# Kernel optimization log

Hardware: AMD Instinct MI355X
Metric: run time of the kernel (lower is better)

## Reference

```python
import jax, jax.numpy as jnp
import numpy as np

N = 50000      # nodes
E = 800000     # edges
FEAT = 128     # node_feat_size
HID = 128      # hidden_channels
LAT = 64       # latent_size
G = 256        # number of graphs in the batch


def _glorot_like(key, fan_in, shape):
    s = 1.0 / np.sqrt(fan_in)
    return jax.random.uniform(key, shape, jnp.float32, -s, s)


def setup_inputs() -> dict:
    key = jax.random.key(0)
    ks = jax.random.split(key, 13)
    x = jax.random.normal(ks[0], (N, FEAT), jnp.float32)
    edge_index = jax.random.randint(ks[1], (2, E), 0, N, dtype=jnp.int64)
    batch = jnp.sort(jax.random.randint(ks[2], (N,), 0, G, dtype=jnp.int64))
    return {
        "x": x,
        "edge_index": edge_index,
        "batch": batch,
        # GCNConv1: FEAT -> HID
        "W1": _glorot_like(ks[3], FEAT, (FEAT, HID)), "b1": jnp.zeros((HID,), jnp.float32),
        # GCNConv2: HID -> HID
        "W2": _glorot_like(ks[4], HID, (HID, HID)), "b2": jnp.zeros((HID,), jnp.float32),
        # fc: HID -> LAT
        "fcW": _glorot_like(ks[5], HID, (HID, LAT)), "fcb": _glorot_like(ks[6], HID, (LAT,)),
        # decoder: LAT -> HID
        "decW": _glorot_like(ks[7], LAT, (LAT, HID)), "decb": _glorot_like(ks[8], LAT, (HID,)),
        # GCNConv3: HID -> FEAT
        "W3": _glorot_like(ks[9], HID, (HID, FEAT)), "b3": jnp.zeros((FEAT,), jnp.float32),
    }


def reference(x, edge_index, batch, W1, b1, W2, b2, fcW, fcb, decW, decb, W3, b3):
    # --- GCN normalization with self-loops (computed once, shared by all convs) ---
    loop = jnp.arange(N, dtype=edge_index.dtype)
    row = jnp.concatenate([edge_index[0], loop])   # source nodes [E+N]
    col = jnp.concatenate([edge_index[1], loop])   # target nodes [E+N]
    deg = jax.ops.segment_sum(jnp.ones(row.shape, x.dtype), col, num_segments=N)
    dinv = jnp.where(deg > 0, jax.lax.rsqrt(deg), jnp.zeros_like(deg))
    norm = dinv[row] * dinv[col]                   # [E+N]

    def gcn(h, W, b):
        h = h @ W                                   # [N, out] transform first (PyG order)
        msg = h[row] * norm[:, None]                # gather + scale, [E+N, out]
        out = jax.ops.segment_sum(msg, col, num_segments=N)  # scatter-add
        return out + b

    # --- encode ---
    h = jax.nn.relu(gcn(x, W1, b1))
    h = jax.nn.relu(gcn(h, W2, b2))
    pooled = jax.ops.segment_sum(h, batch, num_segments=G)   # global_add_pool [G, HID]
    latent = jax.nn.relu(pooled @ fcW + fcb)                 # [G, LAT]

    # --- decode ---
    z = jax.nn.relu(latent @ decW + decb)                    # [G, HID]
    z = z[batch]                                             # broadcast back to nodes [N, HID]
    recon = gcn(z, W3, b3)                                   # [N, FEAT]
    return recon, latent
```

## Files before the change

### kernel.cpp

```cpp
#include <hip/hip_runtime.h>
#include <hip/hip_fp16.h>

static constexpr int NN   = 50000;
static constexpr int EE   = 800000;
static constexpr int GG   = 256;
static constexpr int PCH  = 16;
static constexpr int BK   = 128;
static constexpr int NB   = (NN + BK - 1) / BK;
static constexpr int CAP  = 4096;
static constexpr int CH   = 2048;
static constexpr int ABLK = (EE + CH - 1) / CH;

typedef _Float16 f16;
typedef f16  f16x8 __attribute__((ext_vector_type(8)));
typedef float f32x4 __attribute__((ext_vector_type(4)));

__device__ __forceinline__ int lowerb(const int* __restrict__ b, int n, int v) {
    int lo = 0, hi = n;
    while (lo < hi) { int m = (lo + hi) >> 1; if (b[m] < v) lo = m + 1; else hi = m; }
    return lo;
}

__global__ __launch_bounds__(256) void prep_k(const float* __restrict__ W1,
                                              const float* __restrict__ W2,
                                              f16x8* __restrict__ whi1, f16x8* __restrict__ wlo1,
                                              f16x8* __restrict__ whi2, f16x8* __restrict__ wlo2,
                                              int* __restrict__ bcur,
                                              float* __restrict__ pooled)
{
    int blk = blockIdx.x, t = threadIdx.x;
    if (blk < 16) {
        const float* W = (blk < 8) ? W1 : W2;
        f16x8* wh = (blk < 8) ? whi1 : whi2;
        f16x8* wl = (blk < 8) ? wlo1 : wlo2;
        int tid = (blk & 7) * 256 + t;
        int m  = tid & 15;
        int kq = (tid >> 4) & 3;
        int ks = (tid >> 6) & 3;
        int nt = tid >> 8;
        int n  = nt * 16 + m;
        int k0 = ks * 32 + kq * 8;
        f16x8 h8, l8;
        #pragma unroll
        for (int u = 0; u < 8; u++) {
            float x = W[(size_t)(k0 + u) * 128 + n];
            f16 h = (f16)x;
            h8[u] = h;
            l8[u] = (f16)(x - (float)h);
        }
        wh[tid] = h8;
        wl[tid] = l8;
    } else if (blk == 16) {
        for (int b = t; b < NB; b += 256) bcur[b] = b * CAP;
    } else {
        float4* p = (float4*)pooled;
        for (int j = (blk - 17) * 256 + t; j < GG * 32; j += 512)
            p[j] = make_float4(0.f, 0.f, 0.f, 0.f);
    }
}

__global__ __launch_bounds__(512) void binA_k(const int* __restrict__ ei,
                                              int* __restrict__ bcur,
                                              int2* __restrict__ eraw)
{
    __shared__ int2  stage[CH];
    __shared__ short sbid[CH];
    __shared__ int   hist[NB], loff[NB], gbase[NB], lcur[NB];
    __shared__ int   sc[512];

    int tid = threadIdx.x;
    int e0 = blockIdx.x * CH;
    int n = EE - e0; if (n > CH) n = CH;

    for (int b = tid; b < NB; b += 512) hist[b] = 0;
    __syncthreads();

    int2 r[CH / 512];
    #pragma unroll
    for (int k = 0; k < CH / 512; k++) {
        int s = k * 512 + tid;
        if (s < n) {
            int src = ei[e0 + s];
            int dst = ei[EE + e0 + s];
            r[k] = make_int2(src, dst);
            atomicAdd(&hist[dst >> 7], 1);
        }
    }
    __syncthreads();
    int v = (tid < NB) ? hist[tid] : 0;
    sc[tid] = v;
    __syncthreads();
    #pragma unroll
    for (int off = 1; off < 512; off <<= 1) {
        int add = (tid >= off) ? sc[tid - off] : 0;
        __syncthreads();
        sc[tid] += add;
        __syncthreads();
    }
    if (tid < NB) { int ex = sc[tid] - v; loff[tid] = ex; lcur[tid] = ex; }
    __syncthreads();
    for (int b = tid; b < NB; b += 512)
        gbase[b] = atomicAdd(&bcur[b], hist[b]);
    __syncthreads();
    #pragma unroll
    for (int k = 0; k < CH / 512; k++) {
        int s = k * 512 + tid;
        if (s < n) {
            int b = r[k].y >> 7;
            int slot = atomicAdd(&lcur[b], 1);
            stage[slot] = r[k];
            sbid[slot]  = (short)b;
        }
    }
    __syncthreads();
    for (int s = tid; s < n; s += 512) {
        int b = sbid[s];
        eraw[(size_t)gbase[b] + (s - loff[b])] = stage[s];
    }
}

__global__ __launch_bounds__(512) void scanb2_k(const int* __restrict__ bcur,
                                                int* __restrict__ bbase,
                                                int* __restrict__ rowptr)
{
    __shared__ int s[512];
    int t = threadIdx.x;
    int v = (t < NB) ? (bcur[t] - t * CAP) : 0;
    s[t] = v;
    __syncthreads();
    #pragma unroll
    for (int off = 1; off < 512; off <<= 1) {
        int add = (t >= off) ? s[t - off] : 0;
        __syncthreads();
        s[t] += add;
        __syncthreads();
    }
    if (t < NB) bbase[t] = s[t] - v;
    if (t == 0) rowptr[NN] = EE;
}

__global__ __launch_bounds__(512) void binB_k(const int2* __restrict__ eraw,
                                              const int* __restrict__ bcur,
                                              const int* __restrict__ bbase,
                                              int* __restrict__ rowptr,
                                              float* __restrict__ dinv,
                                              int* __restrict__ ebuf)
{
    __shared__ int hist[BK], excl[BK], cur[BK];
    int b = blockIdx.x, tid = threadIdx.x;
    int t0 = b << 7;
    int lim = NN - t0; if (lim > BK) lim = BK;
    int tot  = bcur[b] - b * CAP;
    int base = bbase[b];
    const int2* er = eraw + (size_t)b * CAP;

    if (tid < BK) hist[tid] = 0;
    __syncthreads();
    for (int s = tid; s < tot; s += 512) atomicAdd(&hist[er[s].y & 127], 1);
    __syncthreads();
    if (tid < BK) excl[tid] = hist[tid];
    __syncthreads();
    #pragma unroll
    for (int off = 1; off < BK; off <<= 1) {
        int add = (tid >= off && tid < BK) ? excl[tid - off] : 0;
        __syncthreads();
        if (tid < BK) excl[tid] += add;
        __syncthreads();
    }
    if (tid < BK) {
        int ex = excl[tid] - hist[tid];
        cur[tid] = base + ex;
        if (tid < lim) {
            rowptr[t0 + tid] = base + ex;
            dinv[t0 + tid]   = rsqrtf((float)(hist[tid] + 1));
        }
    }
    __syncthreads();
    for (int s = tid; s < tot; s += 512) {
        int2 rec = er[s];
        int p = atomicAdd(&cur[rec.y & 127], 1);
        ebuf[p] = rec.x;
    }
}

__global__ void pbb_k(const int* __restrict__ ebuf, const int* __restrict__ batch,
                      const float* __restrict__ dinv, int2* __restrict__ ebuf2)
{
    int e = blockIdx.x * 256 + threadIdx.x;
    if (e < EE) {
        int src = ebuf[e];
        ebuf2[e] = make_int2(batch[src], __float_as_int(dinv[src]));
    }
}

__global__ __launch_bounds__(256) void gemm_mfma3_k(const float* __restrict__ in,
                                                    const f16x8* __restrict__ whi_f,
                                                    const f16x8* __restrict__ wlo_f,
                                                    const float* __restrict__ dinv,
                                                    __half* __restrict__ out,
                                                    int rows)
{
    __shared__ __align__(16) f16x8 sh[2048];
    int tid  = threadIdx.x;
    #pragma unroll
    for (int u = 0; u < 8; u++) sh[u * 256 + tid] = whi_f[u * 256 + tid];
    __syncthreads();

    int lane = tid & 63;
    int wv   = tid >> 6;
    int rB   = blockIdx.x * 64 + wv * 16;
    int m    = lane & 15;
    int kq   = lane >> 4;
    int r    = rB + m;
    int rr   = (r < rows) ? r : (rows - 1);

    f16x8 ahi[4], alo[4];
    const float* rp = in + (size_t)rr * 128 + kq * 8;
    #pragma unroll
    for (int ks = 0; ks < 4; ks++) {
        float4 p0 = *(const float4*)(rp + ks * 32);
        float4 p1 = *(const float4*)(rp + ks * 32 + 4);
        float xs[8] = {p0.x, p0.y, p0.z, p0.w, p1.x, p1.y, p1.z, p1.w};
        #pragma unroll
        for (int u = 0; u < 8; u++) {
            f16 h = (f16)xs[u];
            ahi[ks][u] = h;
            alo[ks][u] = (f16)(xs[u] - (float)h);
        }
    }

    f32x4 acc[8];
    #pragma unroll
    for (int n = 0; n < 8; n++) acc[n] = (f32x4){0.f, 0.f, 0.f, 0.f};

    #pragma unroll
    for (int nt = 0; nt < 8; nt++) {
        #pragma unroll
        for (int ks = 0; ks < 4; ks++) {
            int idx = ((nt * 4 + ks) * 4 + kq) * 16 + m;
            f16x8 bh = sh[idx];
            f16x8 bl = wlo_f[idx];
            acc[nt] = __builtin_amdgcn_mfma_f32_16x16x32_f16(ahi[ks], bh, acc[nt], 0, 0, 0);
            acc[nt] = __builtin_amdgcn_mfma_f32_16x16x32_f16(alo[ks], bh, acc[nt], 0, 0, 0);
            acc[nt] = __builtin_amdgcn_mfma_f32_16x16x32_f16(ahi[ks], bl, acc[nt], 0, 0, 0);
        }
    }

    int   orow[4];
    float dv[4];
    #pragma unroll
    for (int j = 0; j < 4; j++) {
        int gr = rB + kq * 4 + j;
        orow[j] = gr;
        dv[j]   = (gr < rows) ? dinv[gr] : 0.f;
    }
    #pragma unroll
    for (int nt = 0; nt < 8; nt++) {
        int c = nt * 16 + m;
        #pragma unroll
        for (int j = 0; j < 4; j++) {
            if (orow[j] < rows)
                out[(size_t)orow[j] * 128 + c] = __float2half(acc[nt][j] * dv[j]);
        }
    }
}

__device__ __forceinline__ float4 gat4h(const __half* __restrict__ t, int s, int q)
{
    uint2 v = *(const uint2*)(t + ((size_t)s << 7) + q * 4);
    __half2 a = __builtin_bit_cast(__half2, v.x);
    __half2 b = __builtin_bit_cast(__half2, v.y);
    float2 fa = __half22float2(a), fb = __half22float2(b);
    return make_float4(fa.x, fa.y, fb.x, fb.y);
}

__global__ __launch_bounds__(64) void aggh_k(const __half* __restrict__ t,
                                             const int* __restrict__ rowptr,
                                             const int* __restrict__ ebuf,
                                             const float* __restrict__ dinv,
                                             const float* __restrict__ bias,
                                             float* __restrict__ out,
                                             int relu)
{
    int i    = blockIdx.x;
    int lane = threadIdx.x;
    int half = lane >> 5;
    int q    = lane & 31;

    int e0 = __builtin_amdgcn_readfirstlane(rowptr[i]);
    int e1 = __builtin_amdgcn_readfirstlane(rowptr[i + 1]);
    int deg = e1 - e0;
    int idxsafe = (deg > 0) ? (e0 + min(lane, deg - 1)) : 0;
    int myidx = ebuf[idxsafe];

    float a0 = 0.f, a1 = 0.f, a2 = 0.f, a3 = 0.f;
    if (half == 0) {
        float4 v = gat4h(t, i, q);
        a0 = v.x; a1 = v.y; a2 = v.z; a3 = v.w;
    }

    int v   = min(deg, 64);
    int c16 = v & ~15;
    for (int j = half * 8; j < c16; j += 16) {
        int s0 = __shfl(myidx, j + 0), s1 = __shfl(myidx, j + 1);
        int s2 = __shfl(myidx, j + 2), s3 = __shfl(myidx, j + 3);
        int s4 = __shfl(myidx, j + 4), s5 = __shfl(myidx, j + 5);
        int s6 = __shfl(myidx, j + 6), s7 = __shfl(myidx, j + 7);
        float4 w0 = gat4h(t, s0, q);
        float4 w1 = gat4h(t, s1, q);
        float4 w2 = gat4h(t, s2, q);
        float4 w3 = gat4h(t, s3, q);
        float4 w4 = gat4h(t, s4, q);
        float4 w5 = gat4h(t, s5, q);
        float4 w6 = gat4h(t, s6, q);
        float4 w7 = gat4h(t, s7, q);
        a0 += w0.x + w1.x + w2.x + w3.x + w4.x + w5.x + w6.x + w7.x;
        a1 += w0.y + w1.y + w2.y + w3.y + w4.y + w5.y + w6.y + w7.y;
        a2 += w0.z + w1.z + w2.z + w3.z + w4.z + w5.z + w6.z + w7.z;
        a3 += w0.w + w1.w + w2.w + w3.w + w4.w + w5.w + w6.w + w7.w;
    }
    if (v - c16 >= 8) {
        int j = c16 + half * 4;
        int s0 = __shfl(myidx, j + 0), s1 = __shfl(myidx, j + 1);
        int s2 = __shfl(myidx, j + 2), s3 = __shfl(myidx, j + 3);
        float4 w0 = gat4h(t, s0, q);
        float4 w1 = gat4h(t, s1, q);
        float4 w2 = gat4h(t, s2, q);
        float4 w3 = gat4h(t, s3, q);
        a0 += w0.x + w1.x + w2.x + w3.x;
        a1 += w0.y + w1.y + w2.y + w3.y;
        a2 += w0.z + w1.z + w2.z + w3.z;
        a3 += w0.w + w1.w + w2.w + w3.w;
    }
    int done = c16 + ((v - c16) & 8);
    for (int j = done + half; j < v; j += 2) {
        int s = __shfl(myidx, j);
        float4 w = gat4h(t, s, q);
        a0 += w.x; a1 += w.y; a2 += w.z; a3 += w.w;
    }
    for (int e = e0 + 64 + half; e < e1; e += 2) {
        float4 w = gat4h(t, ebuf[e], q);
        a0 += w.x; a1 += w.y; a2 += w.z; a3 += w.w;
    }

    a0 += __shfl_xor(a0, 32);
    a1 += __shfl_xor(a1, 32);
    a2 += __shfl_xor(a2, 32);
    a3 += __shfl_xor(a3, 32);

    if (half == 0) {
        float di = dinv[i];
        float4 b = *(const float4*)(bias + q * 4);
        float4 o;
        o.x = di * a0 + b.x;
        o.y = di * a1 + b.y;
        o.z = di * a2 + b.z;
        o.w = di * a3 + b.w;
        if (relu) {
            o.x = fmaxf(o.x, 0.f); o.y = fmaxf(o.y, 0.f);
            o.z = fmaxf(o.z, 0.f); o.w = fmaxf(o.w, 0.f);
        }
        *(float4*)(out + (size_t)i * 128 + q * 4) = o;
    }
}

__global__ __launch_bounds__(64) void agg_out_k(const float* __restrict__ zz,
                                                const int* __restrict__ batch,
                                                const int* __restrict__ rowptr,
                                                const int2* __restrict__ ebuf2,
                                                const float* __restrict__ dinv,
                                                const float* __restrict__ bias,
                                                float* __restrict__ out)
{
    int i    = blockIdx.x;
    int lane = threadIdx.x;
    int half = lane >> 5;
    int q    = lane & 31;
    float di = dinv[i];

    float a0 = 0.f, a1 = 0.f, a2 = 0.f, a3 = 0.f;
    if (half == 0) {
        float4 v = *(const float4*)(zz + ((size_t)batch[i] << 7) + q * 4);
        a0 = di * v.x; a1 = di * v.y; a2 = di * v.z; a3 = di * v.w;
    }

    int e0 = rowptr[i], e1 = rowptr[i + 1];
    int deg = e1 - e0;
    int full = deg & ~7;
    int ee = e0 + full;
    for (int e = e0 + half * 4; e < ee; e += 8) {
        int2 r0 = ebuf2[e],     r1 = ebuf2[e + 1];
        int2 r2 = ebuf2[e + 2], r3 = ebuf2[e + 3];
        float4 w0 = *(const float4*)(zz + ((size_t)r0.x << 7) + q * 4);
        float4 w1 = *(const float4*)(zz + ((size_t)r1.x << 7) + q * 4);
        float4 w2 = *(const float4*)(zz + ((size_t)r2.x << 7) + q * 4);
        float4 w3 = *(const float4*)(zz + ((size_t)r3.x << 7) + q * 4);
        float n0 = __int_as_float(r0.y), n1 = __int_as_float(r1.y);
        float n2 = __int_as_float(r2.y), n3 = __int_as_float(r3.y);
        a0 += n0 * w0.x + n1 * w1.x + n2 * w2.x + n3 * w3.x;
        a1 += n0 * w0.y + n1 * w1.y + n2 * w2.y + n3 * w3.y;
        a2 += n0 * w0.z + n1 * w1.z + n2 * w2.z + n3 * w3.z;
        a3 += n0 * w0.w + n1 * w1.w + n2 * w2.w + n3 * w3.w;
    }
    for (int e = ee + half; e < e1; e += 2) {
        int2 r = ebuf2[e];
        float nm = __int_as_float(r.y);
        float4 w = *(const float4*)(zz + ((size_t)r.x << 7) + q * 4);
        a0 += nm * w.x; a1 += nm * w.y; a2 += nm * w.z; a3 += nm * w.w;
    }
    a0 += __shfl_xor(a0, 32);
    a1 += __shfl_xor(a1, 32);
    a2 += __shfl_xor(a2, 32);
    a3 += __shfl_xor(a3, 32);

    if (half == 0) {
        float4 b = *(const float4*)(bias + q * 4);
        float4 o;
        o.x = di * a0 + b.x;
        o.y = di * a1 + b.y;
        o.z = di * a2 + b.z;
        o.w = di * a3 + b.w;
        *(float4*)(out + (size_t)i * 128 + q * 4) = o;
    }
}

__global__ __launch_bounds__(128) void pool2_k(const float* __restrict__ h2,
                                               const int* __restrict__ batch,
                                               float* __restrict__ pooled)
{
    int g = blockIdx.x;
    int c = blockIdx.y;
    int f = threadIdx.x;
    int bs = lowerb(batch, NN, g);
    int be = lowerb(batch, NN, g + 1);
    int len = be - bs;
    int cs = bs + (int)(((long long)len * c) / PCH);
    int ce = bs + (int)(((long long)len * (c + 1)) / PCH);
    float a = 0.f;
    for (int i = cs; i < ce; i++) a += h2[(size_t)i * 128 + f];
    if (ce > cs) atomicAdd(&pooled[(size_t)g * 128 + f], a);
}

__global__ __launch_bounds__(128) void fcdec_k(const float* __restrict__ pooled,
                                               const float* __restrict__ fcW,
                                               const float* __restrict__ fcb,
                                               const float* __restrict__ decW,
                                               const float* __restrict__ decb,
                                               const float* __restrict__ W3,
                                               float* __restrict__ lat_out,
                                               float* __restrict__ zz)
{
    __shared__ float lat[64];
    __shared__ float zs[128];
    int g = blockIdx.x, c = threadIdx.x;
    if (c < 64) {
        const float* p = pooled + (size_t)g * 128;
        float a = fcb[c];
        #pragma unroll 8
        for (int k = 0; k < 128; k++) a = fmaf(p[k], fcW[(size_t)k * 64 + c], a);
        a = fmaxf(a, 0.f);
        lat[c] = a;
        lat_out[(size_t)g * 64 + c] = a;
    }
    __syncthreads();
    {
        float a = decb[c];
        #pragma unroll 8
        for (int k = 0; k < 64; k++) a = fmaf(lat[k], decW[(size_t)k * 128 + c], a);
        zs[c] = fmaxf(a, 0.f);
    }
    __syncthreads();
    float o = 0.f;
    #pragma unroll 8
    for (int k = 0; k < 128; k++) o = fmaf(zs[k], W3[(size_t)k * 128 + c], o);
    zz[(size_t)g * 128 + c] = o;
}

extern "C" void kernel_launch(void* const* d_in, const int* in_sizes, int n_in,
                              void* d_out, int out_size, void* d_ws, size_t ws_size,
                              hipStream_t stream)
{
    const float* x     = (const float*)d_in[0];
    const int*   ei    = (const int*)d_in[1];
    const int*   batch = (const int*)d_in[2];
    const float* W1  = (const float*)d_in[3];
    const float* b1  = (const float*)d_in[4];
    const float* W2  = (const float*)d_in[5];
    const float* b2  = (const float*)d_in[6];
    const float* fcW = (const float*)d_in[7];
    const float* fcb = (const float*)d_in[8];
    const float* decW= (const float*)d_in[9];
    const float* decb= (const float*)d_in[10];
    const float* W3  = (const float*)d_in[11];
    const float* b3  = (const float*)d_in[12];

    char* ws = (char*)d_ws;
    size_t off = 0;
    auto alloc = [&](size_t bytes) -> char* {
        char* p = ws + off;
        off = (off + bytes + 255) & ~(size_t)255;
        return p;
    };
    float* dinv     = (float*)alloc((size_t)NN * 4);
    int*   rowptr   = (int*)alloc((size_t)(NN + 1) * 4);
    int*   bcur     = (int*)alloc((size_t)NB * 4);
    int*   bbase    = (int*)alloc((size_t)NB * 4);
    int*   ebuf     = (int*)alloc((size_t)EE * 4);
    int2*  ebuf2    = (int2*)alloc((size_t)EE * 8);
    float* pooled   = (float*)alloc((size_t)GG * 128 * 4);
    float* zz       = (float*)alloc((size_t)GG * 128 * 4);
    f16x8* whi1     = (f16x8*)alloc(2048 * 16);
    f16x8* wlo1     = (f16x8*)alloc(2048 * 16);
    f16x8* whi2     = (f16x8*)alloc(2048 * 16);
    f16x8* wlo2     = (f16x8*)alloc(2048 * 16);
    __half* A       = (__half*)alloc((size_t)NN * 128 * 2);
    float* B        = (float*)alloc((size_t)NN * 128 * 4);
    int2*  eraw     = (int2*)B;

    float* recon_out = (float*)d_out;
    float* lat_out   = (float*)d_out + (size_t)NN * 128;

    prep_k<<<19, 256, 0, stream>>>(W1, W2, whi1, wlo1, whi2, wlo2, bcur, pooled);
    binA_k<<<ABLK, 512, 0, stream>>>(ei, bcur, eraw);
    scanb2_k<<<1, 512, 0, stream>>>(bcur, bbase, rowptr);
    binB_k<<<NB, 512, 0, stream>>>(eraw, bcur, bbase, rowptr, dinv, ebuf);
    pbb_k<<<(EE + 255) / 256, 256, 0, stream>>>(ebuf, batch, dinv, ebuf2);

    int gblk = (NN + 63) / 64;
    gemm_mfma3_k<<<gblk, 256, 0, stream>>>(x, whi1, wlo1, dinv, A, NN);
    aggh_k<<<NN, 64, 0, stream>>>(A, rowptr, ebuf, dinv, b1, B, 1);
    gemm_mfma3_k<<<gblk, 256, 0, stream>>>(B, whi2, wlo2, dinv, A, NN);
    aggh_k<<<NN, 64, 0, stream>>>(A, rowptr, ebuf, dinv, b2, B, 1);
    pool2_k<<<dim3(GG, PCH), 128, 0, stream>>>(B, batch, pooled);
    fcdec_k<<<GG, 128, 0, stream>>>(pooled, fcW, fcb, decW, decb, W3, lat_out, zz);
    agg_out_k<<<NN, 64, 0, stream>>>(zz, batch, rowptr, ebuf2, dinv,
                                     b3, recon_out);
}
```

Measured before the change: 286.1 us.

## Fuse global add pool into second aggregation and fold edge prep into first

The second GCN aggregation now atomically adds its ReLU outputs straight into the per-graph pooled buffer, so the fp32 node-feature write and the separate pool kernel with its binary searches are gone. The per-edge batch/dinv precompute is appended as extra blocks of the first aggregation launch, removing one launch. The cost is 4 float atomics per lane per node into only 256 graph rows, which can cause heavy atomic contention, and the pooled sums are no longer accumulated in a fixed order.

Measured after the change: 361.5 us. 1.26x slower.

```diff
diff --git a/kernel.cpp b/kernel.cpp
--- a/kernel.cpp
+++ b/kernel.cpp
@@ -4,22 +4,16 @@
 static constexpr int NN   = 50000;
 static constexpr int EE   = 800000;
 static constexpr int GG   = 256;
-static constexpr int PCH  = 16;
 static constexpr int BK   = 128;
 static constexpr int NB   = (NN + BK - 1) / BK;
 static constexpr int CAP  = 4096;
 static constexpr int CH   = 2048;
 static constexpr int ABLK = (EE + CH - 1) / CH;
+static constexpr int PBBB = EE / 64;
 
 typedef _Float16 f16;
 typedef f16  f16x8 __attribute__((ext_vector_type(8)));
 typedef float f32x4 __attribute__((ext_vector_type(4)));
-
-__device__ __forceinline__ int lowerb(const int* __restrict__ b, int n, int v) {
-    int lo = 0, hi = n;
-    while (lo < hi) { int m = (lo + hi) >> 1; if (b[m] < v) lo = m + 1; else hi = m; }
-    return lo;
-}
 
 __global__ __launch_bounds__(256) void prep_k(const float* __restrict__ W1,
                                               const float* __restrict__ W2,
@@ -183,16 +177,6 @@
     }
 }
 
-__global__ void pbb_k(const int* __restrict__ ebuf, const int* __restrict__ batch,
-                      const float* __restrict__ dinv, int2* __restrict__ ebuf2)
-{
-    int e = blockIdx.x * 256 + threadIdx.x;
-    if (e < EE) {
-        int src = ebuf[e];
-        ebuf2[e] = make_int2(batch[src], __float_as_int(dinv[src]));
-    }
-}
-
 __global__ __launch_bounds__(256) void gemm_mfma3_k(const float* __restrict__ in,
                                                     const f16x8* __restrict__ whi_f,
                                                     const f16x8* __restrict__ wlo_f,
@@ -274,93 +258,125 @@
     return make_float4(fa.x, fa.y, fb.x, fb.y);
 }
 
+#define AGG_BODY                                                                 \
+    int e0 = __builtin_amdgcn_readfirstlane(rowptr[i]);                          \
+    int e1 = __builtin_amdgcn_readfirstlane(rowptr[i + 1]);                      \
+    int deg = e1 - e0;                                                           \
+    int idxsafe = (deg > 0) ? (e0 + min(lane, deg - 1)) : 0;                     \
+    int myidx = ebuf[idxsafe];                                                   \
+    float a0 = 0.f, a1 = 0.f, a2 = 0.f, a3 = 0.f;                                \
+    if (half == 0) {                                                             \
+        float4 v = gat4h(t, i, q);                                               \
+        a0 = v.x; a1 = v.y; a2 = v.z; a3 = v.w;                                  \
+    }                                                                            \
+    int v   = min(deg, 64);                                                      \
+    int c16 = v & ~15;                                                           \
+    for (int j = half * 8; j < c16; j += 16) {                                   \
+        int s0 = __shfl(myidx, j + 0), s1 = __shfl(myidx, j + 1);                \
+        int s2 = __shfl(myidx, j + 2), s3 = __shfl(myidx, j + 3);                \
+        int s4 = __shfl(myidx, j + 4), s5 = __shfl(myidx, j + 5);                \
+        int s6 = __shfl(myidx, j + 6), s7 = __shfl(myidx, j + 7);                \
+        float4 w0 = gat4h(t, s0, q);                                             \
+        float4 w1 = gat4h(t, s1, q);                                             \
+        float4 w2 = gat4h(t, s2, q);                                             \
+        float4 w3 = gat4h(t, s3, q);                                             \
+        float4 w4 = gat4h(t, s4, q);                                             \
+        float4 w5 = gat4h(t, s5, q);                                             \
+        float4 w6 = gat4h(t, s6, q);                                             \
+        float4 w7 = gat4h(t, s7, q);                                             \
+        a0 += w0.x + w1.x + w2.x + w3.x + w4.x + w5.x + w6.x + w7.x;             \
+        a1 += w0.y + w1.y + w2.y + w3.y + w4.y + w5.y + w6.y + w7.y;             \
+        a2 += w0.z + w1.z + w2.z + w3.z + w4.z + w5.z + w6.z + w7.z;             \
+        a3 += w0.w + w1.w + w2.w + w3.w + w4.w + w5.w + w6.w + w7.w;             \
+    }                                                                            \
+    if (v - c16 >= 8) {                                                          \
+        int j = c16 + half * 4;                                                  \
+        int s0 = __shfl(myidx, j + 0), s1 = __shfl(myidx, j + 1);                \
+        int s2 = __shfl(myidx, j + 2), s3 = __shfl(myidx, j + 3);                \
+        float4 w0 = gat4h(t, s0, q);                                             \
+        float4 w1 = gat4h(t, s1, q);                                             \
+        float4 w2 = gat4h(t, s2, q);                                             \
+        float4 w3 = gat4h(t, s3, q);                                             \
+        a0 += w0.x + w1.x + w2.x + w3.x;                                         \
+        a1 += w0.y + w1.y + w2.y + w3.y;                                         \
+        a2 += w0.z + w1.z + w2.z + w3.z;                                         \
+        a3 += w0.w + w1.w + w2.w + w3.w;                                         \
+    }                                                                            \
+    int done = c16 + ((v - c16) & 8);                                            \
+    for (int j = done + half; j < v; j += 2) {                                   \
+        int s = __shfl(myidx, j);                                                \
+        float4 w = gat4h(t, s, q);                                               \
+        a0 += w.x; a1 += w.y; a2 += w.z; a3 += w.w;                              \
+    }                                                                            \
+    for (int e = e0 + 64 + half; e < e1; e += 2) {                               \
+        float4 w = gat4h(t, ebuf[e], q);                                         \
+        a0 += w.x; a1 += w.y; a2 += w.z; a3 += w.w;                              \
+    }                                                                            \
+    a0 += __shfl_xor(a0, 32);                                                    \
+    a1 += __shfl_xor(a1, 32);                                                    \
+    a2 += __shfl_xor(a2, 32);                                                    \
+    a3 += __shfl_xor(a3, 32);
+
 __global__ __launch_bounds__(64) void aggh_k(const __half* __restrict__ t,
                                              const int* __restrict__ rowptr,
                                              const int* __restrict__ ebuf,
                                              const float* __restrict__ dinv,
                                              const float* __restrict__ bias,
                                              float* __restrict__ out,
-                                             int relu)
+                                             const int* __restrict__ batch,
+                                             int2* __restrict__ ebuf2)
+{
+    int bid  = blockIdx.x;
+    int lane = threadIdx.x;
+    if (bid >= NN) {
+        int e = (bid - NN) * 64 + lane;
+        if (e < EE) {
+            int src = ebuf[e];
+            ebuf2[e] = make_int2(batch[src], __float_as_int(dinv[src]));
+        }
+        return;
+    }
+    int i    = bid;
+    int half = lane >> 5;
+    int q    = lane & 31;
+    AGG_BODY
+    if (half == 0) {
+        float di = dinv[i];
+        float4 b = *(const float4*)(bias + q * 4);
+        float4 o;
+        o.x = fmaxf(di * a0 + b.x, 0.f);
+        o.y = fmaxf(di * a1 + b.y, 0.f);
+        o.z = fmaxf(di * a2 + b.z, 0.f);
+        o.w = fmaxf(di * a3 + b.w, 0.f);
+        *(float4*)(out + (size_t)i * 128 + q * 4) = o;
+    }
+}
+
+__global__ __launch_bounds__(64) void aggh_pool_k(const __half* __restrict__ t,
+                                                  const int* __restrict__ rowptr,
+                                                  const int* __restrict__ ebuf,
+                                                  const float* __restrict__ dinv,
+                                                  const float* __restrict__ bias,
+                                                  const int* __restrict__ batch,
+                                                  float* __restrict__ pooled)
 {
     int i    = blockIdx.x;
     int lane = threadIdx.x;
     int half = lane >> 5;
     int q    = lane & 31;
-
-    int e0 = __builtin_amdgcn_readfirstlane(rowptr[i]);
-    int e1 = __builtin_amdgcn_readfirstlane(rowptr[i + 1]);
-    int deg = e1 - e0;
-    int idxsafe = (deg > 0) ? (e0 + min(lane, deg - 1)) : 0;
-    int myidx = ebuf[idxsafe];
-
-    float a0 = 0.f, a1 = 0.f, a2 = 0.f, a3 = 0.f;
-    if (half == 0) {
-        float4 v = gat4h(t, i, q);
-        a0 = v.x; a1 = v.y; a2 = v.z; a3 = v.w;
-    }
-
-    int v   = min(deg, 64);
-    int c16 = v & ~15;
-    for (int j = half * 8; j < c16; j += 16) {
-        int s0 = __shfl(myidx, j + 0), s1 = __shfl(myidx, j + 1);
-        int s2 = __shfl(myidx, j + 2), s3 = __shfl(myidx, j + 3);
-        int s4 = __shfl(myidx, j + 4), s5 = __shfl(myidx, j + 5);
-        int s6 = __shfl(myidx, j + 6), s7 = __shfl(myidx, j + 7);
-        float4 w0 = gat4h(t, s0, q);
-        float4 w1 = gat4h(t, s1, q);
-        float4 w2 = gat4h(t, s2, q);
-        float4 w3 = gat4h(t, s3, q);
-        float4 w4 = gat4h(t, s4, q);
-        float4 w5 = gat4h(t, s5, q);
-        float4 w6 = gat4h(t, s6, q);
-        float4 w7 = gat4h(t, s7, q);
-        a0 += w0.x + w1.x + w2.x + w3.x + w4.x + w5.x + w6.x + w7.x;
-        a1 += w0.y + w1.y + w2.y + w3.y + w4.y + w5.y + w6.y + w7.y;
-        a2 += w0.z + w1.z + w2.z + w3.z + w4.z + w5.z + w6.z + w7.z;
-        a3 += w0.w + w1.w + w2.w + w3.w + w4.w + w5.w + w6.w + w7.w;
-    }
-    if (v - c16 >= 8) {
-        int j = c16 + half * 4;
-        int s0 = __shfl(myidx, j + 0), s1 = __shfl(myidx, j + 1);
-        int s2 = __shfl(myidx, j + 2), s3 = __shfl(myidx, j + 3);
-        float4 w0 = gat4h(t, s0, q);
-        float4 w1 = gat4h(t, s1, q);
-        float4 w2 = gat4h(t, s2, q);
-        float4 w3 = gat4h(t, s3, q);
-        a0 += w0.x + w1.x + w2.x + w3.x;
-        a1 += w0.y + w1.y + w2.y + w3.y;
-        a2 += w0.z + w1.z + w2.z + w3.z;
-        a3 += w0.w + w1.w + w2.w + w3.w;
-    }
-    int done = c16 + ((v - c16) & 8);
-    for (int j = done + half; j < v; j += 2) {
-        int s = __shfl(myidx, j);
-        float4 w = gat4h(t, s, q);
-        a0 += w.x; a1 += w.y; a2 += w.z; a3 += w.w;
-    }
-    for (int e = e0 + 64 + half; e < e1; e += 2) {
-        float4 w = gat4h(t, ebuf[e], q);
-        a0 += w.x; a1 += w.y; a2 += w.z; a3 += w.w;
-    }
-
-    a0 += __shfl_xor(a0, 32);
-    a1 += __shfl_xor(a1, 32);
-    a2 += __shfl_xor(a2, 32);
-    a3 += __shfl_xor(a3, 32);
-
+    AGG_BODY
     if (half == 0) {
         float di = dinv[i];
         float4 b = *(const float4*)(bias + q * 4);
-        float4 o;
-        o.x = di * a0 + b.x;
-        o.y = di * a1 + b.y;
-        o.z = di * a2 + b.z;
-        o.w = di * a3 + b.w;
-        if (relu) {
-            o.x = fmaxf(o.x, 0.f); o.y = fmaxf(o.y, 0.f);
-            o.z = fmaxf(o.z, 0.f); o.w = fmaxf(o.w, 0.f);
-        }
-        *(float4*)(out + (size_t)i * 128 + q * 4) = o;
+        float ox = fmaxf(di * a0 + b.x, 0.f);
+        float oy = fmaxf(di * a1 + b.y, 0.f);
+        float oz = fmaxf(di * a2 + b.z, 0.f);
+        float ow = fmaxf(di * a3 + b.w, 0.f);
+        float* pp = pooled + (size_t)batch[i] * 128 + q * 4;
+        atomicAdd(pp + 0, ox);
+        atomicAdd(pp + 1, oy);
+        atomicAdd(pp + 2, oz);
+        atomicAdd(pp + 3, ow);
     }
 }
 
@@ -422,23 +438,6 @@
         o.w = di * a3 + b.w;
         *(float4*)(out + (size_t)i * 128 + q * 4) = o;
     }
-}
-
-__global__ __launch_bounds__(128) void pool2_k(const float* __restrict__ h2,
-                                               const int* __restrict__ batch,
-                                               float* __restrict__ pooled)
-{
-    int g = blockIdx.x;
-    int c = blockIdx.y;
-    int f = threadIdx.x;
-    int bs = lowerb(batch, NN, g);
-    int be = lowerb(batch, NN, g + 1);
-    int len = be - bs;
-    int cs = bs + (int)(((long long)len * c) / PCH);
-    int ce = bs + (int)(((long long)len * (c + 1)) / PCH);
-    float a = 0.f;
-    for (int i = cs; i < ce; i++) a += h2[(size_t)i * 128 + f];
-    if (ce > cs) atomicAdd(&pooled[(size_t)g * 128 + f], a);
 }
 
 __global__ __launch_bounds__(128) void fcdec_k(const float* __restrict__ pooled,
@@ -524,14 +523,12 @@
     binA_k<<<ABLK, 512, 0, stream>>>(ei, bcur, eraw);
     scanb2_k<<<1, 512, 0, stream>>>(bcur, bbase, rowptr);
     binB_k<<<NB, 512, 0, stream>>>(eraw, bcur, bbase, rowptr, dinv, ebuf);
-    pbb_k<<<(EE + 255) / 256, 256, 0, stream>>>(ebuf, batch, dinv, ebuf2);
 
     int gblk = (NN + 63) / 64;
     gemm_mfma3_k<<<gblk, 256, 0, stream>>>(x, whi1, wlo1, dinv, A, NN);
-    aggh_k<<<NN, 64, 0, stream>>>(A, rowptr, ebuf, dinv, b1, B, 1);
+    aggh_k<<<NN + PBBB, 64, 0, stream>>>(A, rowptr, ebuf, dinv, b1, B, batch, ebuf2);
     gemm_mfma3_k<<<gblk, 256, 0, stream>>>(B, whi2, wlo2, dinv, A, NN);
-    aggh_k<<<NN, 64, 0, stream>>>(A, rowptr, ebuf, dinv, b2, B, 1);
-    pool2_k<<<dim3(GG, PCH), 128, 0, stream>>>(B, batch, pooled);
+    aggh_pool_k<<<NN, 64, 0, stream>>>(A, rowptr, ebuf, dinv, b2, batch, pooled);
     fcdec_k<<<GG, 128, 0, stream>>>(pooled, fcW, fcb, decW, decb, W3, lat_out, zz);
     agg_out_k<<<NN, 64, 0, stream>>>(zz, batch, rowptr, ebuf2, dinv,
                                      b3, recon_out);
```
